# Optimization experiments

Measured on AMD Instinct MI355X. Metric: run time of the kernel, lower is better.

The kernel has to match this reference:

```python
import itertools
import jax, jax.numpy as jnp
import numpy as np

VOLSHAPE = (160, 192, 160)  # D, H, W (SynthSeg-style 3D crop)
NDIMS = 3
BATCH = 4
CHANNELS = 1


def setup_inputs() -> dict:
    key = jax.random.key(0)
    k1, k2 = jax.random.split(key)
    vol = jax.random.normal(k1, (BATCH, *VOLSHAPE, CHANNELS), dtype=jnp.float32)
    # affine near identity: layer treats trf as (roughly) the full 4x4 matrix applied
    # to centered coordinates; affine_to_shift subtracts the centered mesh.
    trf = jnp.eye(NDIMS + 1, dtype=jnp.float32)[None] \
        + 0.05 * jax.random.normal(k2, (BATCH, NDIMS + 1, NDIMS + 1), dtype=jnp.float32)
    return {"vol": vol, "trf": trf}


def _meshgrid(volshape):
    ranges = [jnp.arange(s, dtype=jnp.float32) for s in volshape]
    return jnp.stack(jnp.meshgrid(*ranges, indexing='ij'), axis=-1)  # [D,H,W,3]


def _affine_to_shift(A, volshape):
    # A: [4,4]; faithful to neuron.utils.affine_to_shift with shift_center=True
    mesh = _meshgrid(volshape)                                        # [D,H,W,3]
    center = jnp.array([(s - 1) / 2.0 for s in volshape], dtype=jnp.float32)
    mesh_c = mesh - center                                            # centered mesh
    flat = mesh_c.reshape(-1, NDIMS)                                  # [V,3]
    flat1 = jnp.concatenate([flat, jnp.ones((flat.shape[0], 1), flat.dtype)], axis=1)  # [V,4]
    loc = flat1 @ A[:NDIMS].T                                         # [V,3] = (A[:3] @ mesh^T)^T
    return loc.reshape(*volshape, NDIMS) - mesh_c                     # shift field


def _interpn_linear(vol, loc):
    # vol: [D,H,W,C]; loc: [D,H,W,3] absolute sample locations
    volshape = vol.shape[:-1]
    C = vol.shape[-1]
    max_loc = jnp.array([d - 1 for d in volshape], dtype=jnp.float32)
    loc0 = jnp.floor(loc)
    clipped = jnp.clip(loc, 0.0, max_loc)
    loc0c = jnp.clip(loc0, 0.0, max_loc)
    loc1c = jnp.clip(loc0c + 1.0, 0.0, max_loc)
    d1 = loc1c - clipped           # weight for corner bit 0 (neuron's reversed ordering)
    d0 = 1.0 - d1                  # weight for corner bit 1
    i0 = loc0c.astype(jnp.int32)
    i1 = loc1c.astype(jnp.int32)
    strides = np.array([volshape[1] * volshape[2], volshape[2], 1], dtype=np.int32)
    vol_flat = vol.reshape(-1, C)
    out = jnp.zeros((*volshape, C), dtype=vol.dtype)
    for corner in itertools.product((0, 1), repeat=NDIMS):
        idx = jnp.zeros(volshape, dtype=jnp.int32)
        wt = jnp.ones(volshape, dtype=vol.dtype)
        for d in range(NDIMS):
            ii = (i0 if corner[d] == 0 else i1)[..., d]
            idx = idx + ii * int(strides[d])
            wt = wt * (d1 if corner[d] == 0 else d0)[..., d]
        gathered = vol_flat[idx.reshape(-1)].reshape(*volshape, C)
        out = out + wt[..., None] * gathered
    return out


def reference(vol, trf):
    volshape = vol.shape[1:-1]

    def single(v, A):
        shift = _affine_to_shift(A, volshape)          # affine -> dense shift field
        loc = _meshgrid(volshape) + shift              # transform(): mesh + shift
        return _interpn_linear(v, loc)

    return jax.vmap(single)(vol, trf)
```

## Files before the change

### kernel.cpp

```cpp
#include <hip/hip_runtime.h>

constexpr int D = 160, H = 192, W = 160, B = 4;
constexpr int V  = D * H * W;
constexpr int HW = H * W;

struct DimS { int i0; float w0; };

__device__ __forceinline__ DimS prep(float loc, float maxv, int maxi) {
    float c  = fminf(fmaxf(loc, 0.0f), maxv);
    int  i0  = min((int)c, maxi - 1);
    DimS s;
    s.i0 = i0;
    s.w0 = (float)(i0 + 1) - c;
    return s;
}

__global__ __launch_bounds__(256) void st_affine_kernel(
        const float* __restrict__ vol, const float* __restrict__ trf,
        float* __restrict__ out) {
    const int b = blockIdx.z;
    const int d = blockIdx.y;
    const int hblk = blockIdx.x / 5;
    const int wblk = blockIdx.x - hblk * 5;
    const int w = wblk * 32 + threadIdx.x;
    const int h = hblk * 8  + threadIdx.y;

    const float* __restrict__ A = trf + b * 16;
    const float a00 = A[0], a01 = A[1], a02 = A[2],  a03 = A[3];
    const float a10 = A[4], a11 = A[5], a12 = A[6],  a13 = A[7];
    const float a20 = A[8], a21 = A[9], a22 = A[10], a23 = A[11];

    constexpr float cd = (D - 1) * 0.5f;
    constexpr float ch = (H - 1) * 0.5f;
    constexpr float cw = (W - 1) * 0.5f;

    const float md = (float)d - cd;
    const float mh = (float)h - ch;
    const float mw = (float)w - cw;

    const float ld = cd + fmaf(a00, md, fmaf(a01, mh, fmaf(a02, mw, a03)));
    const float lh = ch + fmaf(a10, md, fmaf(a11, mh, fmaf(a12, mw, a13)));
    const float lw = cw + fmaf(a20, md, fmaf(a21, mh, fmaf(a22, mw, a23)));

    const DimS sd = prep(ld, (float)(D - 1), D - 1);
    const DimS sh = prep(lh, (float)(H - 1), H - 1);
    const DimS sw = prep(lw, (float)(W - 1), W - 1);

    const float* __restrict__ vb = vol + (size_t)b * V;
    const float* p0 = vb + ((sd.i0 * H + sh.i0) * W + sw.i0);

    float2 v00, v01, v10, v11;
    __builtin_memcpy(&v00, p0,          8);
    __builtin_memcpy(&v01, p0 + W,      8);
    __builtin_memcpy(&v10, p0 + HW,     8);
    __builtin_memcpy(&v11, p0 + HW + W, 8);

    const float pd00 = fmaf(sw.w0, v00.x - v00.y, v00.y);
    const float pd01 = fmaf(sw.w0, v01.x - v01.y, v01.y);
    const float pd10 = fmaf(sw.w0, v10.x - v10.y, v10.y);
    const float pd11 = fmaf(sw.w0, v11.x - v11.y, v11.y);

    const float q0 = fmaf(sh.w0, pd00 - pd01, pd01);
    const float q1 = fmaf(sh.w0, pd10 - pd11, pd11);
    const float r  = fmaf(sd.w0, q0 - q1, q1);

    out[(size_t)b * V + (size_t)(d * H + h) * W + w] = r;
}

extern "C" void kernel_launch(void* const* d_in, const int* in_sizes, int n_in,
                              void* d_out, int out_size, void* d_ws, size_t ws_size,
                              hipStream_t stream) {
    const float* vol = (const float*)d_in[0];
    const float* trf = (const float*)d_in[1];
    float* out = (float*)d_out;

    dim3 grid((H / 8) * (W / 32), D, B);
    dim3 block(32, 8, 1);
    st_affine_kernel<<<grid, block, 0, stream>>>(vol, trf, out);
}
```

Before: 178.5 us.

## Stage source bounding box in shared memory and compute four depth slices per block

Each block now handles four consecutive depth slices. It computes the bounding box of source voxels its affine footprint can touch and cooperatively loads that box into LDS with batched coalesced loads, then does the trilinear interpolation from LDS. Output is written with nontemporal stores. If the footprint exceeds the LDS capacity or row width, it falls back to direct global gathers. This aims to cut redundant global gather traffic, at the cost of a sync, 52 KB of LDS per block and possible loading of unused voxels.

```diff
diff --git a/kernel.cpp b/kernel.cpp
--- a/kernel.cpp
+++ b/kernel.cpp
@@ -3,23 +3,48 @@
 constexpr int D = 160, H = 192, W = 160, B = 4;
 constexpr int V  = D * H * W;
 constexpr int HW = H * W;
+constexpr int CAP = 13312;
 
 struct DimS { int i0; float w0; };
 
 __device__ __forceinline__ DimS prep(float loc, float maxv, int maxi) {
     float c  = fminf(fmaxf(loc, 0.0f), maxv);
     int  i0  = min((int)c, maxi - 1);
-    DimS s;
-    s.i0 = i0;
-    s.w0 = (float)(i0 + 1) - c;
+    DimS s; s.i0 = i0; s.w0 = (float)(i0 + 1) - c;
     return s;
+}
+
+__device__ __forceinline__ int i0_range(float lo, float hi, float maxv, int maxi, int* n) {
+    int iLo = min((int)fminf(fmaxf(lo, 0.0f), maxv), maxi - 1);
+    int iHi = min((int)fminf(fmaxf(hi, 0.0f), maxv), maxi - 1);
+    *n = iHi - iLo + 2;
+    return iLo;
+}
+
+__device__ __forceinline__ float trilerp_g(const float* __restrict__ vb,
+                                           DimS sd, DimS sh, DimS sw) {
+    const float* p0 = vb + ((sd.i0 * H + sh.i0) * W + sw.i0);
+    float2 v00, v01, v10, v11;
+    __builtin_memcpy(&v00, p0,          8);
+    __builtin_memcpy(&v01, p0 + W,      8);
+    __builtin_memcpy(&v10, p0 + HW,     8);
+    __builtin_memcpy(&v11, p0 + HW + W, 8);
+    const float pd00 = fmaf(sw.w0, v00.x - v00.y, v00.y);
+    const float pd01 = fmaf(sw.w0, v01.x - v01.y, v01.y);
+    const float pd10 = fmaf(sw.w0, v10.x - v10.y, v10.y);
+    const float pd11 = fmaf(sw.w0, v11.x - v11.y, v11.y);
+    const float q0 = fmaf(sh.w0, pd00 - pd01, pd01);
+    const float q1 = fmaf(sh.w0, pd10 - pd11, pd11);
+    return fmaf(sd.w0, q0 - q1, q1);
 }
 
 __global__ __launch_bounds__(256) void st_affine_kernel(
         const float* __restrict__ vol, const float* __restrict__ trf,
         float* __restrict__ out) {
-    const int b = blockIdx.z;
-    const int d = blockIdx.y;
+    __shared__ float smem[CAP];
+
+    const int b  = blockIdx.z;
+    const int d0 = blockIdx.y * 4;
     const int hblk = blockIdx.x / 5;
     const int wblk = blockIdx.x - hblk * 5;
     const int w = wblk * 32 + threadIdx.x;
@@ -34,37 +59,100 @@
     constexpr float ch = (H - 1) * 0.5f;
     constexpr float cw = (W - 1) * 0.5f;
 
-    const float md = (float)d - cd;
-    const float mh = (float)h - ch;
-    const float mw = (float)w - cw;
+    const float mdc = (float)d0 + 1.5f - cd;
+    const float mhc = (float)(hblk * 8)  + 3.5f  - ch;
+    const float mwc = (float)(wblk * 32) + 15.5f - cw;
+    const float lcD = cd + fmaf(a00, mdc, fmaf(a01, mhc, fmaf(a02, mwc, a03)));
+    const float lcH = ch + fmaf(a10, mdc, fmaf(a11, mhc, fmaf(a12, mwc, a13)));
+    const float lcW = cw + fmaf(a20, mdc, fmaf(a21, mhc, fmaf(a22, mwc, a23)));
+    const float rD = fabsf(a00) * 1.5f + fabsf(a01) * 3.5f + fabsf(a02) * 15.5f + 0.02f;
+    const float rH = fabsf(a10) * 1.5f + fabsf(a11) * 3.5f + fabsf(a12) * 15.5f + 0.02f;
+    const float rW = fabsf(a20) * 1.5f + fabsf(a21) * 3.5f + fabsf(a22) * 15.5f + 0.02f;
 
-    const float ld = cd + fmaf(a00, md, fmaf(a01, mh, fmaf(a02, mw, a03)));
-    const float lh = ch + fmaf(a10, md, fmaf(a11, mh, fmaf(a12, mw, a13)));
-    const float lw = cw + fmaf(a20, md, fmaf(a21, mh, fmaf(a22, mw, a23)));
-
-    const DimS sd = prep(ld, (float)(D - 1), D - 1);
-    const DimS sh = prep(lh, (float)(H - 1), H - 1);
-    const DimS sw = prep(lw, (float)(W - 1), W - 1);
+    int zn, yn, xn;
+    const int zlo = i0_range(lcD - rD, lcD + rD, (float)(D - 1), D - 1, &zn);
+    const int ylo = i0_range(lcH - rH, lcH + rH, (float)(H - 1), H - 1, &yn);
+    const int xlo = i0_range(lcW - rW, lcW + rW, (float)(W - 1), W - 1, &xn);
+    const bool fits = (xn <= 64) && (zn * yn * xn <= CAP);
 
     const float* __restrict__ vb = vol + (size_t)b * V;
-    const float* p0 = vb + ((sd.i0 * H + sh.i0) * W + sw.i0);
 
-    float2 v00, v01, v10, v11;
-    __builtin_memcpy(&v00, p0,          8);
-    __builtin_memcpy(&v01, p0 + W,      8);
-    __builtin_memcpy(&v10, p0 + HW,     8);
-    __builtin_memcpy(&v11, p0 + HW + W, 8);
+    const float md = (float)d0 - cd;
+    const float mh = (float)h  - ch;
+    const float mw = (float)w  - cw;
+    float ld = cd + fmaf(a00, md, fmaf(a01, mh, fmaf(a02, mw, a03)));
+    float lh = ch + fmaf(a10, md, fmaf(a11, mh, fmaf(a12, mw, a13)));
+    float lw = cw + fmaf(a20, md, fmaf(a21, mh, fmaf(a22, mw, a23)));
 
-    const float pd00 = fmaf(sw.w0, v00.x - v00.y, v00.y);
-    const float pd01 = fmaf(sw.w0, v01.x - v01.y, v01.y);
-    const float pd10 = fmaf(sw.w0, v10.x - v10.y, v10.y);
-    const float pd11 = fmaf(sw.w0, v11.x - v11.y, v11.y);
+    float res[4];
 
-    const float q0 = fmaf(sh.w0, pd00 - pd01, pd01);
-    const float q1 = fmaf(sh.w0, pd10 - pd11, pd11);
-    const float r  = fmaf(sd.w0, q0 - q1, q1);
+    if (fits) {
+        const int t      = threadIdx.y * 32 + threadIdx.x;
+        const int lane   = t & 63;
+        const int waveId = t >> 6;
+        const int R = zn * yn;
+        int zi = 0, yi = waveId;
+        if (yi >= yn) { yi -= yn; ++zi; }
+        int r = waveId;
+        while (r < R) {
+            float vbuf[8];
+            int zi2 = zi, yi2 = yi;
+            #pragma unroll
+            for (int k = 0; k < 8; ++k) {
+                const int rk = r + 4 * k;
+                float val = 0.0f;
+                if (rk < R && lane < xn)
+                    val = vb[(size_t)((zlo + zi2) * H + (ylo + yi2)) * W + xlo + lane];
+                vbuf[k] = val;
+                yi2 += 4;
+                if (yi2 >= yn) { yi2 -= yn; ++zi2; }
+                if (yi2 >= yn) { yi2 -= yn; ++zi2; }
+            }
+            #pragma unroll
+            for (int k = 0; k < 8; ++k) {
+                const int rk = r + 4 * k;
+                if (rk < R && lane < xn) smem[rk * xn + lane] = vbuf[k];
+            }
+            zi = zi2; yi = yi2;
+            r += 32;
+        }
+        __syncthreads();
 
-    out[(size_t)b * V + (size_t)(d * H + h) * W + w] = r;
+        const int pl = yn * xn;
+        #pragma unroll
+        for (int k = 0; k < 4; ++k) {
+            const DimS sd = prep(ld, (float)(D - 1), D - 1);
+            const DimS sh = prep(lh, (float)(H - 1), H - 1);
+            const DimS sw = prep(lw, (float)(W - 1), W - 1);
+            const int base = ((sd.i0 - zlo) * yn + (sh.i0 - ylo)) * xn + (sw.i0 - xlo);
+            const float v00x = smem[base],           v00y = smem[base + 1];
+            const float v01x = smem[base + xn],      v01y = smem[base + xn + 1];
+            const float v10x = smem[base + pl],      v10y = smem[base + pl + 1];
+            const float v11x = smem[base + pl + xn], v11y = smem[base + pl + xn + 1];
+            const float pd00 = fmaf(sw.w0, v00x - v00y, v00y);
+            const float pd01 = fmaf(sw.w0, v01x - v01y, v01y);
+            const float pd10 = fmaf(sw.w0, v10x - v10y, v10y);
+            const float pd11 = fmaf(sw.w0, v11x - v11y, v11y);
+            const float q0 = fmaf(sh.w0, pd00 - pd01, pd01);
+            const float q1 = fmaf(sh.w0, pd10 - pd11, pd11);
+            res[k] = fmaf(sd.w0, q0 - q1, q1);
+            ld += a00; lh += a10; lw += a20;
+        }
+    } else {
+        #pragma unroll
+        for (int k = 0; k < 4; ++k) {
+            const DimS sd = prep(ld, (float)(D - 1), D - 1);
+            const DimS sh = prep(lh, (float)(H - 1), H - 1);
+            const DimS sw = prep(lw, (float)(W - 1), W - 1);
+            res[k] = trilerp_g(vb, sd, sh, sw);
+            ld += a00; lh += a10; lw += a20;
+        }
+    }
+
+    float* ob = out + (size_t)b * V + (size_t)h * W + w;
+    #pragma unroll
+    for (int k = 0; k < 4; ++k)
+        __builtin_nontemporal_store(res[k], ob + (size_t)(d0 + k) * HW);
 }
 
 extern "C" void kernel_launch(void* const* d_in, const int* in_sizes, int n_in,
@@ -74,7 +162,7 @@
     const float* trf = (const float*)d_in[1];
     float* out = (float*)d_out;
 
-    dim3 grid((H / 8) * (W / 32), D, B);
+    dim3 grid((H / 8) * (W / 32), D / 4, B);
     dim3 block(32, 8, 1);
     st_affine_kernel<<<grid, block, 0, stream>>>(vol, trf, out);
 }
```

New measurement: 209.6 us. 1.17x slower.
